# Performance work log

Measured on AMD Instinct MI355X. Metric: run time of the kernel, lower is better.

Reference implementation:

```python
import jax, jax.numpy as jnp
import numpy as np

KERNEL = 3
STRIDE = 1

def _unfold(x, k, s):
    # torch.nn.Unfold: output [B, C*k*k, P] with (c, kh, kw) flattened channel-major
    B, C, H, W = x.shape
    oh = (H - k) // s + 1
    ow = (W - k) // s + 1
    cols = []
    for di in range(k):
        for dj in range(k):
            cols.append(x[:, :, di:di + oh * s:s, dj:dj + ow * s:s])
    p = jnp.stack(cols, axis=2)            # [B, C, k*k, oh, ow]
    return p.reshape(B, C * k * k, oh * ow), oh, ow

def setup_inputs() -> dict:
    key = jax.random.key(0)
    k1, k2 = jax.random.split(key)
    B, C, H, W = 32, 96, 32, 32
    out_c, k, s = 96, KERNEL, STRIDE
    oh = (H - k) // s + 1
    ow = (W - k) // s + 1
    P = oh * ow
    x = jax.random.normal(k1, (B, C, H, W), dtype=jnp.float32)
    weight = jax.random.normal(k2, (P, out_c, C * k * k), dtype=jnp.float32) * 0.01
    bias = jnp.zeros((P, out_c), dtype=jnp.float32)
    return {"x": x, "weight": weight, "bias": bias}

def reference(x, weight, bias):
    B = x.shape[0]
    out_c = weight.shape[1]
    patches, oh, ow = _unfold(x, KERNEL, STRIDE)          # [B, K, P]
    # per-patch distinct weights: out[b,p,o] = sum_k patches[b,k,p] * weight[p,o,k]
    out = jnp.einsum('bkp,pok->bpo', patches, weight) + bias[None, :, :]
    out = out.transpose(0, 2, 1).reshape(B, out_c, oh, ow)
    return out
```

## Files before the change

kernel.cpp:

```cpp
#include <hip/hip_runtime.h>


namespace {
constexpr int CIN  = 96;
constexpr int HW_  = 1024;
constexpr int CSTR = CIN * HW_;
constexpr int OC   = 96;
constexpr int OW   = 30;
constexpr int NP   = 900;
constexpr int KTOT = 864;
constexpr int KC   = 96;
constexpr int NCH  = KTOT / KC;
constexpr int NTHR = 192;
constexpr int NBLK = NP * 2;
}

typedef __attribute__((ext_vector_type(8))) short bf16x8;
typedef __attribute__((ext_vector_type(4))) float f32x4;

__device__ __forceinline__ unsigned f2bf_pk(float lo, float hi) {
    unsigned ul = __builtin_bit_cast(unsigned, lo);
    unsigned uh = __builtin_bit_cast(unsigned, hi);
    ul += 0x7fffu + ((ul >> 16) & 1u);
    uh += 0x7fffu + ((uh >> 16) & 1u);
    return (ul >> 16) | (uh & 0xffff0000u);
}

__global__ __launch_bounds__(NTHR, 4)
void lc_mfma(const float* __restrict__ x, const float* __restrict__ weight,
             const float* __restrict__ bias, float* __restrict__ ws)
{
    __shared__ uint4 Albuf[2][384];

    const int bid = blockIdx.x;
    const int p   = bid >> 1;
    const int oh  = bid & 1;
    const int pi  = p / OW;
    const int pj  = p - pi * OW;

    const int t = threadIdx.x, lane = t & 63, wv = t >> 6;

    const int nlane = lane & 15;
    const int kq    = lane >> 4;
    const int o_ln  = oh * 48 + wv * 16 + nlane;
    const float* wrow = weight + ((size_t)p * OC + o_ln) * KTOT + (kq << 3);
    const float  bb   = bias[(size_t)p * OC + o_ln];

    const int bs = t & 31, kset = t >> 5;
    const int mt = bs >> 4, bl = bs & 15;
    const float* xb = x + (size_t)bs * CSTR + pi * 32 + pj;

    int wr_idx[2];
    #pragma unroll
    for (int w = 0; w < 2; ++w) {
        const int kk0 = 16 * kset + 8 * w;
        wr_idx[w] = ((kk0 >> 5) * 2 + mt) * 64 + bl + (((kk0 & 31) >> 3) << 4);
    }

    f32x4 acc0 = {0.f, 0.f, 0.f, 0.f};
    f32x4 acc1 = {0.f, 0.f, 0.f, 0.f};

    float  xf[16];
    float4 wn[6];

#define XLOAD(CH)                                               \
    _Pragma("unroll")                                           \
    for (int d = 0; d < 16; ++d) {                              \
        const int k  = (CH) * KC + 16 * kset + d;               \
        const int c  = k / 9;                                   \
        const int r  = k - 9 * c;                               \
        const int di = r / 3;                                   \
        const int dj = r - 3 * di;                              \
        xf[d] = xb[c * HW_ + di * 32 + dj];                     \
    }

#define WLOAD(CH)                                                        \
    _Pragma("unroll")                                                    \
    for (int s = 0; s < 3; ++s) {                                        \
        wn[2 * s]     = *(const float4*)(wrow + (CH) * KC + s * 32);     \
        wn[2 * s + 1] = *(const float4*)(wrow + (CH) * KC + s * 32 + 4); \
    }

    XLOAD(0)
    WLOAD(0)

    #pragma unroll
    for (int ch = 0; ch < NCH; ++ch) {
        const uint4 v0 = {f2bf_pk(xf[0], xf[1]),  f2bf_pk(xf[2], xf[3]),
                          f2bf_pk(xf[4], xf[5]),  f2bf_pk(xf[6], xf[7])};
        const uint4 v1 = {f2bf_pk(xf[8], xf[9]),  f2bf_pk(xf[10], xf[11]),
                          f2bf_pk(xf[12], xf[13]), f2bf_pk(xf[14], xf[15])};
        Albuf[ch & 1][wr_idx[0]] = v0;
        Albuf[ch & 1][wr_idx[1]] = v1;

        unsigned wb[12];
        #pragma unroll
        for (int s = 0; s < 3; ++s) {
            wb[4 * s + 0] = f2bf_pk(wn[2 * s].x,     wn[2 * s].y);
            wb[4 * s + 1] = f2bf_pk(wn[2 * s].z,     wn[2 * s].w);
            wb[4 * s + 2] = f2bf_pk(wn[2 * s + 1].x, wn[2 * s + 1].y);
            wb[4 * s + 3] = f2bf_pk(wn[2 * s + 1].z, wn[2 * s + 1].w);
        }

        if (ch < NCH - 1) { XLOAD(ch + 1) WLOAD(ch + 1) }

        __syncthreads();

        const bf16x8* Af = reinterpret_cast<const bf16x8*>(&Albuf[ch & 1][0]);
        #pragma unroll
        for (int s = 0; s < 3; ++s) {
            const bf16x8 bfr = __builtin_bit_cast(bf16x8,
                (uint4){wb[4 * s], wb[4 * s + 1], wb[4 * s + 2], wb[4 * s + 3]});
            const bf16x8 a0 = Af[(s * 2 + 0) * 64 + lane];
            const bf16x8 a1 = Af[(s * 2 + 1) * 64 + lane];
            acc0 = __builtin_amdgcn_mfma_f32_16x16x32_bf16(a0, bfr, acc0, 0, 0, 0);
            acc1 = __builtin_amdgcn_mfma_f32_16x16x32_bf16(a1, bfr, acc1, 0, 0, 0);
        }
    }
#undef XLOAD
#undef WLOAD

    float* wsp = ws + (size_t)p * (32 * OC);
    #pragma unroll
    for (int r = 0; r < 4; ++r) {
        const int brow = (kq << 2) + r;
        wsp[(size_t)brow * OC + o_ln]        = acc0[r] + bb;
        wsp[(size_t)(16 + brow) * OC + o_ln] = acc1[r] + bb;
    }
}

__global__ __launch_bounds__(256)
void lc_transpose(const float* __restrict__ ws, float* __restrict__ out)
{
    __shared__ float tile[64][65];
    const int bo0 = blockIdx.x * 64;
    const int p0  = blockIdx.y * 64;
    const int tx  = threadIdx.x & 63;
    const int ty  = threadIdx.x >> 6;

    #pragma unroll
    for (int i = 0; i < 16; ++i) {
        const int pp = i * 4 + ty;
        if (p0 + pp < NP)
            tile[pp][tx] = ws[(size_t)(p0 + pp) * 3072 + bo0 + tx];
    }
    __syncthreads();
    #pragma unroll
    for (int i = 0; i < 16; ++i) {
        const int bb = i * 4 + ty;
        if (p0 + tx < NP)
            out[(size_t)(bo0 + bb) * NP + p0 + tx] = tile[tx][bb];
    }
}

extern "C" void kernel_launch(void* const* d_in, const int* in_sizes, int n_in,
                              void* d_out, int out_size, void* d_ws, size_t ws_size,
                              hipStream_t stream) {
    const float* x  = (const float*)d_in[0];
    const float* w  = (const float*)d_in[1];
    const float* bi = (const float*)d_in[2];
    float* out      = (float*)d_out;
    float* ws       = (float*)d_ws;

    lc_mfma<<<dim3(NBLK), dim3(NTHR), 0, stream>>>(x, w, bi, ws);
    lc_transpose<<<dim3(3072 / 64, (NP + 63) / 64), dim3(256), 0, stream>>>(ws, out);
}
```

Measured before the change: 535.4 us.

## Split im2col into a separate bf16 pre-pass and stream tiles via global_load_lds

```diff
diff --git a/kernel.cpp b/kernel.cpp
--- a/kernel.cpp
+++ b/kernel.cpp
@@ -9,10 +9,9 @@
 constexpr int OW   = 30;
 constexpr int NP   = 900;
 constexpr int KTOT = 864;
-constexpr int KC   = 96;
-constexpr int NCH  = KTOT / KC;
-constexpr int NTHR = 192;
-constexpr int NBLK = NP * 2;
+constexpr size_t ACOLS_U4    = (size_t)NP * 3456;
+constexpr size_t ACOLS_BYTES = ACOLS_U4 * 16;
+constexpr size_t WS2_BYTES   = (size_t)NP * 32 * OC * 4;
 }
 
 typedef __attribute__((ext_vector_type(8))) short bf16x8;
@@ -26,26 +25,150 @@
     return (ul >> 16) | (uh & 0xffff0000u);
 }
 
-__global__ __launch_bounds__(NTHR, 4)
-void lc_mfma(const float* __restrict__ x, const float* __restrict__ weight,
-             const float* __restrict__ bias, float* __restrict__ ws)
-{
-    __shared__ uint4 Albuf[2][384];
+__global__ __launch_bounds__(256, 2)
+void lc_im2col(const float* __restrict__ x, uint4* __restrict__ Acols)
+{
+    __shared__ unsigned short Xl[16 * 1924];
+    unsigned* Xl32 = (unsigned*)Xl;
 
     const int bid = blockIdx.x;
-    const int p   = bid >> 1;
-    const int oh  = bid & 1;
-    const int pi  = p / OW;
-    const int pj  = p - pi * OW;
+    const int pjh = bid & 1;
+    const int mt  = (bid >> 1) & 1;
+    const int cch = (bid >> 2) % 3;
+    const int pi  = bid / 12;
+    const int c0  = cch * 32;
+    const int w0e = pjh ? 12 : 0;
+    const int pj0 = pjh * 15;
 
     const int t = threadIdx.x, lane = t & 63, wv = t >> 6;
 
-    const int nlane = lane & 15;
-    const int kq    = lane >> 4;
-    const int o_ln  = oh * 48 + wv * 16 + nlane;
+    for (int it = 0; it < 60; ++it) {
+        const int T   = t + it * 256;
+        const int row = T / 10;
+        const int pr  = T - row * 10;
+        const int bl  = row / 96;
+        const int rem = row - bl * 96;
+        const int c   = rem / 3;
+        const int di  = rem - c * 3;
+        const float2 v = *(const float2*)(x + (size_t)(mt * 16 + bl) * CSTR
+                             + (c0 + c) * HW_ + (pi + di) * 32 + w0e + 2 * pr);
+        Xl32[bl * 962 + (c * 3 + di) * 10 + pr] = f2bf_pk(v.x, v.y);
+    }
+    __syncthreads();
+
+    const int khi = lane >> 4, bl = lane & 15;
+    for (int sl = 0; sl < 9; ++sl) {
+        int off[8];
+        #pragma unroll
+        for (int e = 0; e < 8; ++e) {
+            const int kl = 32 * sl + 8 * khi + e;
+            const int c  = (kl * 57) >> 9;
+            const int r  = kl - 9 * c;
+            const int di = (r * 11) >> 5;
+            const int dj = r - 3 * di;
+            off[e] = bl * 1924 + (c * 3 + di) * 20 + dj - w0e;
+        }
+        const int s = cch * 9 + sl;
+        for (int pjl = wv; pjl < 15; pjl += 4) {
+            const int pj = pj0 + pjl;
+            const int p  = pi * OW + pj;
+            unsigned short v0 = Xl[off[0] + pj], v1 = Xl[off[1] + pj];
+            unsigned short v2 = Xl[off[2] + pj], v3 = Xl[off[3] + pj];
+            unsigned short v4 = Xl[off[4] + pj], v5 = Xl[off[5] + pj];
+            unsigned short v6 = Xl[off[6] + pj], v7 = Xl[off[7] + pj];
+            uint4 u;
+            u.x = v0 | ((unsigned)v1 << 16);
+            u.y = v2 | ((unsigned)v3 << 16);
+            u.z = v4 | ((unsigned)v5 << 16);
+            u.w = v6 | ((unsigned)v7 << 16);
+            Acols[(size_t)((p * 27 + s) * 2 + mt) * 64 + lane] = u;
+        }
+    }
+}
+
+__global__ __launch_bounds__(384, 3)
+void lc_mfma6(const float* __restrict__ weight, const float* __restrict__ bias,
+              const uint4* __restrict__ Acols, float* __restrict__ ws2)
+{
+    __shared__ uint4 Albuf[2][1152];
+
+    const int p = blockIdx.x;
+    const int t = threadIdx.x, lane = t & 63, wv = t >> 6;
+    const int nlane = lane & 15, kq = lane >> 4;
+    const int o_ln  = wv * 16 + nlane;
     const float* wrow = weight + ((size_t)p * OC + o_ln) * KTOT + (kq << 3);
     const float  bb   = bias[(size_t)p * OC + o_ln];
-
+    const uint4* ag   = Acols + (size_t)p * 3456 + wv * 64 + lane;
+
+    f32x4 acc0 = {0.f, 0.f, 0.f, 0.f};
+    f32x4 acc1 = {0.f, 0.f, 0.f, 0.f};
+
+#define STAGE(CH, BF)                                                           \
+    {                                                                           \
+        _Pragma("unroll")                                                       \
+        for (int rd = 0; rd < 3; ++rd) {                                        \
+            __builtin_amdgcn_global_load_lds(                                   \
+                (const __attribute__((address_space(1))) unsigned*)             \
+                    (ag + (CH) * 1152 + rd * 384),                              \
+                (__attribute__((address_space(3))) unsigned*)                   \
+                    &Albuf[BF][rd * 384 + wv * 64],                             \
+                16, 0, 0);                                                      \
+        }                                                                       \
+    }
+
+    STAGE(0, 0)
+
+    #pragma unroll
+    for (int ch = 0; ch < 3; ++ch) {
+        __syncthreads();
+        if (ch < 2) STAGE(ch + 1, (ch + 1) & 1)
+
+        float4 wn[18];
+        #pragma unroll
+        for (int s = 0; s < 9; ++s) {
+            wn[2 * s]     = *(const float4*)(wrow + (size_t)ch * 288 + s * 32);
+            wn[2 * s + 1] = *(const float4*)(wrow + (size_t)ch * 288 + s * 32 + 4);
+        }
+        const bf16x8* Af = (const bf16x8*)&Albuf[ch & 1][0];
+        #pragma unroll
+        for (int s = 0; s < 9; ++s) {
+            uint4 wbu;
+            wbu.x = f2bf_pk(wn[2 * s].x,     wn[2 * s].y);
+            wbu.y = f2bf_pk(wn[2 * s].z,     wn[2 * s].w);
+            wbu.z = f2bf_pk(wn[2 * s + 1].x, wn[2 * s + 1].y);
+            wbu.w = f2bf_pk(wn[2 * s + 1].z, wn[2 * s + 1].w);
+            const bf16x8 bfr = __builtin_bit_cast(bf16x8, wbu);
+            const bf16x8 a0  = Af[(s * 2 + 0) * 64 + lane];
+            const bf16x8 a1  = Af[(s * 2 + 1) * 64 + lane];
+            acc0 = __builtin_amdgcn_mfma_f32_16x16x32_bf16(a0, bfr, acc0, 0, 0, 0);
+            acc1 = __builtin_amdgcn_mfma_f32_16x16x32_bf16(a1, bfr, acc1, 0, 0, 0);
+        }
+    }
+#undef STAGE
+
+    float* wsp = ws2 + (size_t)p * (32 * OC);
+    #pragma unroll
+    for (int r = 0; r < 4; ++r) {
+        const int brow = (kq << 2) + r;
+        wsp[(size_t)brow * OC + o_ln]        = acc0[r] + bb;
+        wsp[(size_t)(16 + brow) * OC + o_ln] = acc1[r] + bb;
+    }
+}
+
+__global__ __launch_bounds__(192, 4)
+void lc_mfma_fb(const float* __restrict__ x, const float* __restrict__ weight,
+                const float* __restrict__ bias, float* __restrict__ ws2)
+{
+    __shared__ uint4 Albuf[2][384];
+
+    const int bid = blockIdx.x;
+    const int p = bid >> 1, oh = bid & 1;
+    const int pi = p / OW, pj = p - pi * OW;
+    const int t = threadIdx.x, lane = t & 63, wv = t >> 6;
+    const int nlane = lane & 15, kq = lane >> 4;
+    const int o_ln = oh * 48 + wv * 16 + nlane;
+    const float* wrow = weight + ((size_t)p * OC + o_ln) * KTOT + (kq << 3);
+    const float  bb   = bias[(size_t)p * OC + o_ln];
     const int bs = t & 31, kset = t >> 5;
     const int mt = bs >> 4, bl = bs & 15;
     const float* xb = x + (size_t)bs * CSTR + pi * 32 + pj;
@@ -56,71 +179,58 @@
         const int kk0 = 16 * kset + 8 * w;
         wr_idx[w] = ((kk0 >> 5) * 2 + mt) * 64 + bl + (((kk0 & 31) >> 3) << 4);
     }
-
-    f32x4 acc0 = {0.f, 0.f, 0.f, 0.f};
-    f32x4 acc1 = {0.f, 0.f, 0.f, 0.f};
-
-    float  xf[16];
-    float4 wn[6];
-
-#define XLOAD(CH)                                               \
+    f32x4 acc0 = {0.f,0.f,0.f,0.f}, acc1 = {0.f,0.f,0.f,0.f};
+    float xf[16]; float4 wn[6];
+
+#define XLOADF(CH)                                              \
     _Pragma("unroll")                                           \
     for (int d = 0; d < 16; ++d) {                              \
-        const int k  = (CH) * KC + 16 * kset + d;               \
+        const int k  = (CH) * 96 + 16 * kset + d;               \
         const int c  = k / 9;                                   \
         const int r  = k - 9 * c;                               \
         const int di = r / 3;                                   \
         const int dj = r - 3 * di;                              \
         xf[d] = xb[c * HW_ + di * 32 + dj];                     \
     }
-
-#define WLOAD(CH)                                                        \
+#define WLOADF(CH)                                                       \
     _Pragma("unroll")                                                    \
     for (int s = 0; s < 3; ++s) {                                        \
-        wn[2 * s]     = *(const float4*)(wrow + (CH) * KC + s * 32);     \
-        wn[2 * s + 1] = *(const float4*)(wrow + (CH) * KC + s * 32 + 4); \
-    }
-
-    XLOAD(0)
-    WLOAD(0)
-
-    #pragma unroll
-    for (int ch = 0; ch < NCH; ++ch) {
-        const uint4 v0 = {f2bf_pk(xf[0], xf[1]),  f2bf_pk(xf[2], xf[3]),
-                          f2bf_pk(xf[4], xf[5]),  f2bf_pk(xf[6], xf[7])};
-        const uint4 v1 = {f2bf_pk(xf[8], xf[9]),  f2bf_pk(xf[10], xf[11]),
-                          f2bf_pk(xf[12], xf[13]), f2bf_pk(xf[14], xf[15])};
+        wn[2 * s]     = *(const float4*)(wrow + (CH) * 96 + s * 32);     \
+        wn[2 * s + 1] = *(const float4*)(wrow + (CH) * 96 + s * 32 + 4); \
+    }
+    XLOADF(0) WLOADF(0)
+    #pragma unroll
+    for (int ch = 0; ch < 9; ++ch) {
+        const uint4 v0 = {f2bf_pk(xf[0],xf[1]),  f2bf_pk(xf[2],xf[3]),
+                          f2bf_pk(xf[4],xf[5]),  f2bf_pk(xf[6],xf[7])};
+        const uint4 v1 = {f2bf_pk(xf[8],xf[9]),  f2bf_pk(xf[10],xf[11]),
+                          f2bf_pk(xf[12],xf[13]),f2bf_pk(xf[14],xf[15])};
         Albuf[ch & 1][wr_idx[0]] = v0;
         Albuf[ch & 1][wr_idx[1]] = v1;
-
         unsigned wb[12];
         #pragma unroll
         for (int s = 0; s < 3; ++s) {
-            wb[4 * s + 0] = f2bf_pk(wn[2 * s].x,     wn[2 * s].y);
-            wb[4 * s + 1] = f2bf_pk(wn[2 * s].z,     wn[2 * s].w);
-            wb[4 * s + 2] = f2bf_pk(wn[2 * s + 1].x, wn[2 * s + 1].y);
-            wb[4 * s + 3] = f2bf_pk(wn[2 * s + 1].z, wn[2 * s + 1].w);
-        }
-
-        if (ch < NCH - 1) { XLOAD(ch + 1) WLOAD(ch + 1) }
-
+            wb[4*s+0] = f2bf_pk(wn[2*s].x,   wn[2*s].y);
+            wb[4*s+1] = f2bf_pk(wn[2*s].z,   wn[2*s].w);
+            wb[4*s+2] = f2bf_pk(wn[2*s+1].x, wn[2*s+1].y);
+            wb[4*s+3] = f2bf_pk(wn[2*s+1].z, wn[2*s+1].w);
+        }
+        if (ch < 8) { XLOADF(ch + 1) WLOADF(ch + 1) }
         __syncthreads();
-
-        const bf16x8* Af = reinterpret_cast<const bf16x8*>(&Albuf[ch & 1][0]);
+        const bf16x8* Af = (const bf16x8*)&Albuf[ch & 1][0];
         #pragma unroll
         for (int s = 0; s < 3; ++s) {
             const bf16x8 bfr = __builtin_bit_cast(bf16x8,
-                (uint4){wb[4 * s], wb[4 * s + 1], wb[4 * s + 2], wb[4 * s + 3]});
+                (uint4){wb[4*s], wb[4*s+1], wb[4*s+2], wb[4*s+3]});
             const bf16x8 a0 = Af[(s * 2 + 0) * 64 + lane];
             const bf16x8 a1 = Af[(s * 2 + 1) * 64 + lane];
             acc0 = __builtin_amdgcn_mfma_f32_16x16x32_bf16(a0, bfr, acc0, 0, 0, 0);
             acc1 = __builtin_amdgcn_mfma_f32_16x16x32_bf16(a1, bfr, acc1, 0, 0, 0);
         }
     }
-#undef XLOAD
-#undef WLOAD
-
-    float* wsp = ws + (size_t)p * (32 * OC);
+#undef XLOADF
+#undef WLOADF
+    float* wsp = ws2 + (size_t)p * (32 * OC);
     #pragma unroll
     for (int r = 0; r < 4; ++r) {
         const int brow = (kq << 2) + r;
@@ -130,19 +240,18 @@
 }
 
 __global__ __launch_bounds__(256)
-void lc_transpose(const float* __restrict__ ws, float* __restrict__ out)
+void lc_transpose(const float* __restrict__ ws2, float* __restrict__ out)
 {
     __shared__ float tile[64][65];
     const int bo0 = blockIdx.x * 64;
     const int p0  = blockIdx.y * 64;
     const int tx  = threadIdx.x & 63;
     const int ty  = threadIdx.x >> 6;
-
     #pragma unroll
     for (int i = 0; i < 16; ++i) {
         const int pp = i * 4 + ty;
         if (p0 + pp < NP)
-            tile[pp][tx] = ws[(size_t)(p0 + pp) * 3072 + bo0 + tx];
+            tile[pp][tx] = ws2[(size_t)(p0 + pp) * 3072 + bo0 + tx];
     }
     __syncthreads();
     #pragma unroll
@@ -160,8 +269,16 @@
     const float* w  = (const float*)d_in[1];
     const float* bi = (const float*)d_in[2];
     float* out      = (float*)d_out;
-    float* ws       = (float*)d_ws;
-
-    lc_mfma<<<dim3(NBLK), dim3(NTHR), 0, stream>>>(x, w, bi, ws);
-    lc_transpose<<<dim3(3072 / 64, (NP + 63) / 64), dim3(256), 0, stream>>>(ws, out);
-}
+
+    if (ws_size >= ACOLS_BYTES + WS2_BYTES) {
+        uint4* Acols = (uint4*)d_ws;
+        float* ws2   = (float*)((char*)d_ws + ACOLS_BYTES);
+        lc_im2col<<<dim3(360), dim3(256), 0, stream>>>(x, Acols);
+        lc_mfma6<<<dim3(NP), dim3(384), 0, stream>>>(w, bi, Acols, ws2);
+        lc_transpose<<<dim3(3072 / 64, (NP + 63) / 64), dim3(256), 0, stream>>>(ws2, out);
+    } else {
+        float* ws2 = (float*)d_ws;
+        lc_mfma_fb<<<dim3(NP * 2), dim3(192), 0, stream>>>(x, w, bi, ws2);
+        lc_transpose<<<dim3(3072 / 64, (NP + 63) / 64), dim3(256), 0, stream>>>(ws2, out);
+    }
+}
```

Measured after the change: 450.1 us. 1.19x faster.
